# Kernel optimization log

Measured on AMD Instinct MI355X. Metric: run time of the kernel, lower is better.

## Reference

```python
import jax, jax.numpy as jnp
import numpy as np

N = 100000   # nodes per type
E = 400000   # edges per relation
D = 128      # in_dim == out_dim
H = 4        # heads
DK = D // H  # 32
EPS = 1e-5


def setup_inputs() -> dict:
    key = jax.random.key(0)
    ks = jax.random.split(key, 16)
    s = 1.0 / np.sqrt(D)  # fan-in scaling for stable activations
    inp = {
        "x_drug": jax.random.normal(ks[0], (N, D), jnp.float32),
        "x_dis": jax.random.normal(ks[1], (N, D), jnp.float32),
        "Wp_drug": jax.random.normal(ks[2], (D, D), jnp.float32) * s,
        "bp_drug": jnp.zeros((D,), jnp.float32),
        "Wp_dis": jax.random.normal(ks[3], (D, D), jnp.float32) * s,
        "bp_dis": jnp.zeros((D,), jnp.float32),
        "Wk_r0": jax.random.normal(ks[4], (D, D), jnp.float32) * s,
        "Wv_r0": jax.random.normal(ks[5], (D, D), jnp.float32) * s,
        "Wk_r1": jax.random.normal(ks[6], (D, D), jnp.float32) * s,
        "Wv_r1": jax.random.normal(ks[7], (D, D), jnp.float32) * s,
        "Wu_drug": jax.random.normal(ks[8], (D, D), jnp.float32) * s,
        "bu_drug": jnp.zeros((D,), jnp.float32),
        "Wu_dis": jax.random.normal(ks[9], (D, D), jnp.float32) * s,
        "bu_dis": jnp.zeros((D,), jnp.float32),
        "g_drug": jnp.ones((D,), jnp.float32),
        "be_drug": jnp.zeros((D,), jnp.float32),
        "g_dis": jnp.ones((D,), jnp.float32),
        "be_dis": jnp.zeros((D,), jnp.float32),
        "ei_r0": jax.random.randint(ks[10], (2, E), 0, N, jnp.int32),  # drug -> dis
        "ei_r1": jax.random.randint(ks[11], (2, E), 0, N, jnp.int32),  # dis  -> drug
    }
    return inp


def _rel_attention(h_src_all, h_dst_all, ei, Wk, Wv, n_dst):
    # gather -> per-relation K/V proj -> edge softmax over dst -> scatter-add
    src, dst = ei[0], ei[1]
    h_src = h_src_all[src]                                  # [E, D]
    Q = h_dst_all[dst].reshape(-1, H, DK)                   # [E, H, DK]
    K = (h_src @ Wk).reshape(-1, H, DK)
    V = (h_src @ Wv).reshape(-1, H, DK)
    scores = jnp.sum(Q * K, axis=-1) / np.sqrt(DK)          # [E, H]
    # scatter_softmax over destination groups (numerically stable)
    m = jax.lax.stop_gradient(
        jax.ops.segment_max(scores, dst, num_segments=n_dst))  # [N, H]
    ex = jnp.exp(scores - m[dst])
    ssum = jax.ops.segment_sum(ex, dst, num_segments=n_dst)    # [N, H]
    attn = ex / ssum[dst]                                      # [E, H]
    wV = (V * attn[..., None]).reshape(-1, D)                  # [E, D]
    return jax.ops.segment_sum(wV, dst, num_segments=n_dst)    # [N, D]


def _update(h, agg, Wu, bu, g, be):
    x = h + (agg @ Wu + bu)  # skip + update (dropout=0)
    mu = jnp.mean(x, axis=-1, keepdims=True)
    var = jnp.var(x, axis=-1, keepdims=True)
    ln = (x - mu) * jax.lax.rsqrt(var + EPS) * g + be
    return jax.nn.relu(ln)


def reference(x_drug, x_dis, Wp_drug, bp_drug, Wp_dis, bp_dis,
              Wk_r0, Wv_r0, Wk_r1, Wv_r1,
              Wu_drug, bu_drug, Wu_dis, bu_dis,
              g_drug, be_drug, g_dis, be_dis, ei_r0, ei_r1):
    # type-specific projection
    h_drug = x_drug @ Wp_drug + bp_drug
    h_dis = x_dis @ Wp_dis + bp_dis
    # per-relation attention + intra/inter-type aggregation
    agg_dis = _rel_attention(h_drug, h_dis, ei_r0, Wk_r0, Wv_r0, N)
    agg_drug = _rel_attention(h_dis, h_drug, ei_r1, Wk_r1, Wv_r1, N)
    out_drug = _update(h_drug, agg_drug, Wu_drug, bu_drug, g_drug, be_drug)
    out_dis = _update(h_dis, agg_dis, Wu_dis, bu_dis, g_dis, be_dis)
    return jnp.stack([out_drug, out_dis])  # [2, N, D]
```

## Files before the change

### kernel.cpp

```cpp
#include <hip/hip_runtime.h>
#include <math.h>

#define NN 100000
#define EE 400000
#define DD 128

typedef __attribute__((ext_vector_type(8))) short bf16x8;
typedef __attribute__((ext_vector_type(4))) float f32x4;

#if defined(__has_builtin)
#if __has_builtin(__builtin_amdgcn_fdot2_f32_bf16)
#define HAVE_FDOT2 1
typedef __attribute__((ext_vector_type(2))) __bf16 bf16x2t;
#endif
#endif

__device__ __forceinline__ unsigned short f2bf(float f) {
  unsigned u = __float_as_uint(f);
  u += 0x7FFF + ((u >> 16) & 1);
  return (unsigned short)(u >> 16);
}
__device__ __forceinline__ float bf2f(unsigned short u) {
  return __uint_as_float(((unsigned)u) << 16);
}

__global__ __launch_bounds__(256) void prep_weights(
    const float* __restrict__ Wp_dr, const float* __restrict__ bp_dr,
    const float* __restrict__ Wp_di, const float* __restrict__ bp_di,
    const float* __restrict__ Wu_dr, const float* __restrict__ Wu_di,
    const float* __restrict__ Bk0, const float* __restrict__ Bv0,
    const float* __restrict__ Bk1, const float* __restrict__ Bv1,
    unsigned short* __restrict__ Wpt_dr, unsigned short* __restrict__ Wpt_di,
    unsigned short* __restrict__ Wut_dr, unsigned short* __restrict__ Wut_di,
    unsigned short* __restrict__ Wkt0, float* __restrict__ bk0,
    unsigned short* __restrict__ Wvt0, float* __restrict__ bv0,
    unsigned short* __restrict__ Wkt1, float* __restrict__ bk1,
    unsigned short* __restrict__ Wvt1, float* __restrict__ bv1,
    int* __restrict__ deg) {
  const int b = blockIdx.x, t = threadIdx.x;
  if (b < 256) {
    const int id = b * 256 + t;
    const int m = id >> 14, rem = id & 16383, k = rem & 127, c = rem >> 7;
    const float* W = (m == 0) ? Wp_dr : (m == 1) ? Wp_di : (m == 2) ? Wu_dr : Wu_di;
    unsigned short* O = (m == 0) ? Wpt_dr : (m == 1) ? Wpt_di : (m == 2) ? Wut_dr : Wut_di;
    O[c * DD + k] = f2bf(W[(size_t)k * DD + c]);
  } else if (b < 512) {
    const int id = (b - 256) * 256 + t;
    const int m = id >> 14, rem = id & 16383, k = rem & 127, c = rem >> 7;
    const float* A = (m < 2) ? Wp_dr : Wp_di;
    const float* B = (m == 0) ? Bk0 : (m == 1) ? Bv0 : (m == 2) ? Bk1 : Bv1;
    unsigned short* O = (m == 0) ? Wkt0 : (m == 1) ? Wvt0 : (m == 2) ? Wkt1 : Wvt1;
    const float4* a4 = (const float4*)(A + (size_t)k * DD);
    float s = 0.0f;
#pragma unroll 8
    for (int j4 = 0; j4 < 32; ++j4) {
      const float4 av = a4[j4];
      s += av.x * B[(4 * j4 + 0) * DD + c] + av.y * B[(4 * j4 + 1) * DD + c]
         + av.z * B[(4 * j4 + 2) * DD + c] + av.w * B[(4 * j4 + 3) * DD + c];
    }
    O[c * DD + k] = f2bf(s);
  } else if (b < 514) {
    const int id = (b - 512) * 256 + t;
    if (id < 512) {
      const int m = id >> 7, c = id & 127;
      const float* bp = (m < 2) ? bp_dr : bp_di;
      const float* B = (m == 0) ? Bk0 : (m == 1) ? Bv0 : (m == 2) ? Bk1 : Bv1;
      float* bo = (m == 0) ? bk0 : (m == 1) ? bv0 : (m == 2) ? bk1 : bv1;
      float s = 0.0f;
#pragma unroll 8
      for (int j = 0; j < DD; ++j) s += bp[j] * B[j * DD + c];
      bo[c] = s;
    }
  } else {
    const int id = (b - 514) * 256 + t;
    if (id < 2 * NN) deg[id] = 0;
  }
}

#define STAGE_W(SRC)                                                          \
  do {                                                                        \
    __syncthreads();                                                          \
    _Pragma("unroll") for (int i_ = threadIdx.x; i_ < 2048; i_ += 256) {      \
      const int L_ = i_ * 16;                                                 \
      *(float4*)((char*)WL + (L_ ^ (((L_ >> 8) & 15) << 4))) =                \
          ((const float4*)(SRC))[i_];                                         \
    }                                                                         \
    __syncthreads();                                                          \
  } while (0)

__device__ __forceinline__ void mfma_tile_store(
    const unsigned short* WL, const bf16x8* a, int lane, int rowbase,
    bool wvalid, const float* __restrict__ bias,
    unsigned short* __restrict__ outb) {
  const int r0 = rowbase + (lane >> 4) * 4;
#pragma unroll
  for (int ni = 0; ni < 8; ++ni) {
    const int cl = ni * 16 + (lane & 15);
    f32x4 acc = {0.f, 0.f, 0.f, 0.f};
#pragma unroll
    for (int kk = 0; kk < 4; ++kk) {
      const int boff = cl * 256 + ((kk * 64 + (lane >> 4) * 16) ^ ((cl & 15) << 4));
      const bf16x8 bb = *(const bf16x8*)((const char*)WL + boff);
      acc = __builtin_amdgcn_mfma_f32_16x16x32_bf16(a[kk], bb, acc, 0, 0, 0);
    }
    if (wvalid) {
      const float bv = bias[cl];
#pragma unroll
      for (int r = 0; r < 4; ++r)
        outb[(size_t)(r0 + r) * DD + cl] = f2bf(acc[r] + bv);
    }
  }
}

__global__ __launch_bounds__(256) void fused_proj(
    const float* __restrict__ x0, const unsigned short* __restrict__ Wpt0,
    const float* __restrict__ bp0, const unsigned short* __restrict__ Wkta,
    const float* __restrict__ bka, const unsigned short* __restrict__ Wvta,
    const float* __restrict__ bva, unsigned short* __restrict__ h0,
    unsigned short* __restrict__ K0, unsigned short* __restrict__ V0,
    const float* __restrict__ x1, const unsigned short* __restrict__ Wpt1,
    const float* __restrict__ bp1, const unsigned short* __restrict__ Wktb,
    const float* __restrict__ bkb, const unsigned short* __restrict__ Wvtb,
    const float* __restrict__ bvb, unsigned short* __restrict__ h1,
    unsigned short* __restrict__ K1, unsigned short* __restrict__ V1,
    int half, int cntblocks,
    const int* __restrict__ ei0, const int* __restrict__ ei1,
    int* __restrict__ deg) {
  __shared__ unsigned short WL[DD * DD];
  int bid = blockIdx.x;
  if (bid < cntblocks) {
    const int e = bid * 256 + threadIdx.x;
    if (e < 2 * EE) {
      const int d = (e < EE) ? ei0[EE + e] : (NN + ei1[e]);
      atomicAdd(&deg[d], 1);
    }
    return;
  }
  bid -= cntblocks;
  const bool second = bid >= half;
  if (second) bid -= half;
  const float* x = second ? x1 : x0;
  const unsigned short* Wpt = second ? Wpt1 : Wpt0;
  const float* bpv = second ? bp1 : bp0;
  const unsigned short* Wkt = second ? Wktb : Wkta;
  const float* bkv = second ? bkb : bka;
  const unsigned short* Wvt = second ? Wvtb : Wvta;
  const float* bvv = second ? bvb : bva;
  unsigned short* h = second ? h1 : h0;
  unsigned short* K = second ? K1 : K0;
  unsigned short* V = second ? V1 : V0;

  const int tid = threadIdx.x, lane = tid & 63, wid = tid >> 6;
  const int rowbase = bid * 64 + wid * 16;
  const bool wvalid = rowbase < NN;
  bf16x8 a[4];
  if (wvalid) {
    const int arow = rowbase + (lane & 15);
    const float* xr = x + (size_t)arow * DD + (lane >> 4) * 8;
#pragma unroll
    for (int kk = 0; kk < 4; ++kk) {
      const float4 f0 = *(const float4*)(xr + kk * 32);
      const float4 f1 = *(const float4*)(xr + kk * 32 + 4);
      a[kk][0] = (short)f2bf(f0.x); a[kk][1] = (short)f2bf(f0.y);
      a[kk][2] = (short)f2bf(f0.z); a[kk][3] = (short)f2bf(f0.w);
      a[kk][4] = (short)f2bf(f1.x); a[kk][5] = (short)f2bf(f1.y);
      a[kk][6] = (short)f2bf(f1.z); a[kk][7] = (short)f2bf(f1.w);
    }
  } else {
#pragma unroll
    for (int kk = 0; kk < 4; ++kk)
#pragma unroll
      for (int j = 0; j < 8; ++j) a[kk][j] = 0;
  }
  STAGE_W(Wpt);
  mfma_tile_store(WL, a, lane, rowbase, wvalid, bpv, h);
  STAGE_W(Wkt);
  mfma_tile_store(WL, a, lane, rowbase, wvalid, bkv, K);
  STAGE_W(Wvt);
  mfma_tile_store(WL, a, lane, rowbase, wvalid, bvv, V);
}

__global__ __launch_bounds__(256) void update_ln2(
    const unsigned short* __restrict__ hA, const unsigned short* __restrict__ aggA,
    const unsigned short* __restrict__ WutA, const float* __restrict__ buA,
    const float* __restrict__ gA, const float* __restrict__ beA,
    float* __restrict__ outA,
    const unsigned short* __restrict__ hB, const unsigned short* __restrict__ aggB,
    const unsigned short* __restrict__ WutB, const float* __restrict__ buB,
    const float* __restrict__ gB, const float* __restrict__ beB,
    float* __restrict__ outB, int half) {
  __shared__ unsigned short WL[DD * DD];
  int bid = blockIdx.x;
  const bool second = bid >= half;
  if (second) bid -= half;
  const unsigned short* h = second ? hB : hA;
  const unsigned short* agg = second ? aggB : aggA;
  const unsigned short* Wut = second ? WutB : WutA;
  const float* bu = second ? buB : buA;
  const float* g = second ? gB : gA;
  const float* be = second ? beB : beA;
  float* out = second ? outB : outA;

  const int tid = threadIdx.x, lane = tid & 63, wid = tid >> 6;
  const int rowbase = bid * 64 + wid * 16;
  const bool wvalid = rowbase < NN;
  bf16x8 a[4];
  if (wvalid) {
    const int arow = rowbase + (lane & 15);
#pragma unroll
    for (int kk = 0; kk < 4; ++kk)
      a[kk] = *(const bf16x8*)(agg + (size_t)arow * DD + kk * 32 + (lane >> 4) * 8);
  } else {
#pragma unroll
    for (int kk = 0; kk < 4; ++kk)
#pragma unroll
      for (int j = 0; j < 8; ++j) a[kk][j] = 0;
  }
#pragma unroll
  for (int i_ = tid; i_ < 2048; i_ += 256) {
    const int L_ = i_ * 16;
    *(float4*)((char*)WL + (L_ ^ (((L_ >> 8) & 15) << 4))) =
        ((const float4*)Wut)[i_];
  }
  __syncthreads();
  f32x4 acc[8];
  const int r0 = rowbase + (lane >> 4) * 4;
#pragma unroll
  for (int ni = 0; ni < 8; ++ni) {
    const int cl = ni * 16 + (lane & 15);
    acc[ni] = (f32x4){0.f, 0.f, 0.f, 0.f};
#pragma unroll
    for (int kk = 0; kk < 4; ++kk) {
      const int boff = cl * 256 + ((kk * 64 + (lane >> 4) * 16) ^ ((cl & 15) << 4));
      const bf16x8 bb = *(const bf16x8*)((const char*)WL + boff);
      acc[ni] = __builtin_amdgcn_mfma_f32_16x16x32_bf16(a[kk], bb, acc[ni], 0, 0, 0);
    }
  }
  if (!wvalid) return;
#pragma unroll
  for (int ni = 0; ni < 8; ++ni) {
    const int cl = ni * 16 + (lane & 15);
    const float bv = bu[cl];
#pragma unroll
    for (int r = 0; r < 4; ++r)
      acc[ni][r] += bf2f(h[(size_t)(r0 + r) * DD + cl]) + bv;
  }
  float mean[4], inv[4];
#pragma unroll
  for (int r = 0; r < 4; ++r) {
    float s = 0.f, q = 0.f;
#pragma unroll
    for (int ni = 0; ni < 8; ++ni) {
      const float v = acc[ni][r];
      s += v; q += v * v;
    }
    s += __shfl_xor(s, 1); q += __shfl_xor(q, 1);
    s += __shfl_xor(s, 2); q += __shfl_xor(q, 2);
    s += __shfl_xor(s, 4); q += __shfl_xor(q, 4);
    s += __shfl_xor(s, 8); q += __shfl_xor(q, 8);
    const float mu = s * (1.0f / 128.0f);
    mean[r] = mu;
    inv[r] = rsqrtf(q * (1.0f / 128.0f) - mu * mu + 1e-5f);
  }
#pragma unroll
  for (int ni = 0; ni < 8; ++ni) {
    const int cl = ni * 16 + (lane & 15);
    const float gv = g[cl], bev = be[cl];
#pragma unroll
    for (int r = 0; r < 4; ++r)
      out[(size_t)(r0 + r) * DD + cl] =
          fmaxf((acc[ni][r] - mean[r]) * inv[r] * gv + bev, 0.0f);
  }
}

__global__ __launch_bounds__(256) void scan1(const int* __restrict__ deg,
                                             int* __restrict__ excl,
                                             int* __restrict__ partials, int n) {
  __shared__ int ls[256];
  const int b0 = blockIdx.x * 1024;
  const int t = threadIdx.x;
  int v[4];
  int s = 0;
#pragma unroll
  for (int i = 0; i < 4; ++i) {
    const int idx = b0 + t * 4 + i;
    v[i] = (idx < n) ? deg[idx] : 0;
    s += v[i];
  }
  ls[t] = s;
  __syncthreads();
  for (int off = 1; off < 256; off <<= 1) {
    const int x = (t >= off) ? ls[t - off] : 0;
    __syncthreads();
    ls[t] += x;
    __syncthreads();
  }
  int ex = ls[t] - s;
#pragma unroll
  for (int i = 0; i < 4; ++i) {
    const int idx = b0 + t * 4 + i;
    if (idx < n) excl[idx] = ex;
    ex += v[i];
  }
  if (t == 255) partials[blockIdx.x] = ls[255];
}

__global__ __launch_bounds__(256) void scan2(int* __restrict__ partials, int nb) {
  __shared__ int ls[256];
  const int t = threadIdx.x;
  const int v = (t < nb) ? partials[t] : 0;
  ls[t] = v;
  __syncthreads();
  for (int off = 1; off < 256; off <<= 1) {
    const int x = (t >= off) ? ls[t - off] : 0;
    __syncthreads();
    ls[t] += x;
    __syncthreads();
  }
  if (t < nb) partials[t] = ls[t] - v;
}

__global__ __launch_bounds__(256) void scan3(const int* __restrict__ excl,
                                             const int* __restrict__ partials,
                                             int n, int* __restrict__ rowptr) {
  const int i = blockIdx.x * 256 + threadIdx.x;
  if (i < n) rowptr[i] = excl[i] + partials[i >> 10];
}

__global__ __launch_bounds__(256) void fill_csr2(const int* __restrict__ ei0,
                                                 const int* __restrict__ ei1,
                                                 int* __restrict__ rowptr,
                                                 int* __restrict__ csr_src) {
  const int e = blockIdx.x * 256 + threadIdx.x;
  if (e >= 2 * EE) return;
  int s, d;
  if (e < EE) { s = ei0[e]; d = ei0[EE + e]; }
  else        { s = ei1[e - EE]; d = NN + ei1[e]; }
  const int p = atomicAdd(&rowptr[d], 1);
  csr_src[p] = s;
}

__global__ __launch_bounds__(256) void dst_attention(
    const unsigned short* __restrict__ Hq0, const unsigned short* __restrict__ K0,
    const unsigned short* __restrict__ V0, unsigned short* __restrict__ agg0,
    const unsigned short* __restrict__ Hq1, const unsigned short* __restrict__ K1,
    const unsigned short* __restrict__ V1, unsigned short* __restrict__ agg1,
    const int* __restrict__ rowptr, const int* __restrict__ deg,
    const int* __restrict__ csr_src) {
  const int gw = blockIdx.x * 4 + (threadIdx.x >> 6);
  if (gw >= 2 * NN) return;
  const bool rel1 = gw >= NN;
  const int node = rel1 ? gw - NN : gw;
  const unsigned short* Hq = rel1 ? Hq1 : Hq0;
  const char* Kb = (const char*)(rel1 ? K1 : K0);
  const char* Vb = (const char*)(rel1 ? V1 : V0);
  unsigned short* agg = rel1 ? agg1 : agg0;

  const int lane = threadIdx.x & 63;
  const int sub = lane & 15;
  const int grp = lane >> 4;
  const unsigned lboff = (unsigned)sub << 4;
  const int end = rowptr[gw];
  const int beg = end - deg[gw];
  const uint4 qu = *(const uint4*)(Hq + (size_t)node * DD + sub * 8);
#if defined(HAVE_FDOT2)
  const bf16x2t q0 = __builtin_bit_cast(bf16x2t, qu.x);
  const bf16x2t q1 = __builtin_bit_cast(bf16x2t, qu.y);
  const bf16x2t q2 = __builtin_bit_cast(bf16x2t, qu.z);
  const bf16x2t q3 = __builtin_bit_cast(bf16x2t, qu.w);
#else
  float qf[8];
  qf[0] = bf2f((unsigned short)qu.x); qf[1] = bf2f((unsigned short)(qu.x >> 16));
  qf[2] = bf2f((unsigned short)qu.y); qf[3] = bf2f((unsigned short)(qu.y >> 16));
  qf[4] = bf2f((unsigned short)qu.z); qf[5] = bf2f((unsigned short)(qu.z >> 16));
  qf[6] = bf2f((unsigned short)qu.w); qf[7] = bf2f((unsigned short)(qu.w >> 16));
#endif
  float av[8] = {0.f, 0.f, 0.f, 0.f, 0.f, 0.f, 0.f, 0.f};
  float lsum = 0.0f;
  for (int i = beg + grp; i < end; i += 4) {
    const unsigned roff = ((unsigned)csr_src[i] << 8) + lboff;
    const uint4 kp = *(const uint4*)(Kb + roff);
#if defined(HAVE_FDOT2)
    float p = __builtin_amdgcn_fdot2_f32_bf16(__builtin_bit_cast(bf16x2t, kp.x), q0, 0.0f, false);
    p = __builtin_amdgcn_fdot2_f32_bf16(__builtin_bit_cast(bf16x2t, kp.y), q1, p, false);
    p = __builtin_amdgcn_fdot2_f32_bf16(__builtin_bit_cast(bf16x2t, kp.z), q2, p, false);
    p = __builtin_amdgcn_fdot2_f32_bf16(__builtin_bit_cast(bf16x2t, kp.w), q3, p, false);
#else
    float p;
    p  = qf[0] * bf2f((unsigned short)kp.x) + qf[1] * bf2f((unsigned short)(kp.x >> 16));
    p += qf[2] * bf2f((unsigned short)kp.y) + qf[3] * bf2f((unsigned short)(kp.y >> 16));
    p += qf[4] * bf2f((unsigned short)kp.z) + qf[5] * bf2f((unsigned short)(kp.z >> 16));
    p += qf[6] * bf2f((unsigned short)kp.w) + qf[7] * bf2f((unsigned short)(kp.w >> 16));
#endif
    p += __shfl_xor(p, 1);
    p += __shfl_xor(p, 2);
    const float wgt = __expf(p * 0.17677669529663689f);
    const uint4 vp = *(const uint4*)(Vb + roff);
    lsum += wgt;
    av[0] += wgt * __uint_as_float(vp.x << 16);
    av[1] += wgt * __uint_as_float(vp.x & 0xFFFF0000u);
    av[2] += wgt * __uint_as_float(vp.y << 16);
    av[3] += wgt * __uint_as_float(vp.y & 0xFFFF0000u);
    av[4] += wgt * __uint_as_float(vp.z << 16);
    av[5] += wgt * __uint_as_float(vp.z & 0xFFFF0000u);
    av[6] += wgt * __uint_as_float(vp.w << 16);
    av[7] += wgt * __uint_as_float(vp.w & 0xFFFF0000u);
  }
#pragma unroll
  for (int d = 0; d < 8; ++d) {
    av[d] += __shfl_xor(av[d], 16);
    av[d] += __shfl_xor(av[d], 32);
  }
  lsum += __shfl_xor(lsum, 16);
  lsum += __shfl_xor(lsum, 32);
  if (grp == 0) {
    const float invl = (lsum > 0.0f) ? (1.0f / lsum) : 0.0f;
    uint4 o;
    o.x = (unsigned)f2bf(av[0] * invl) | ((unsigned)f2bf(av[1] * invl) << 16);
    o.y = (unsigned)f2bf(av[2] * invl) | ((unsigned)f2bf(av[3] * invl) << 16);
    o.z = (unsigned)f2bf(av[4] * invl) | ((unsigned)f2bf(av[5] * invl) << 16);
    o.w = (unsigned)f2bf(av[6] * invl) | ((unsigned)f2bf(av[7] * invl) << 16);
    *(uint4*)(agg + (size_t)node * DD + sub * 8) = o;
  }
}

extern "C" void kernel_launch(void* const* d_in, const int* in_sizes, int n_in,
                              void* d_out, int out_size, void* d_ws, size_t ws_size,
                              hipStream_t stream) {
  const float* x_drug  = (const float*)d_in[0];
  const float* x_dis   = (const float*)d_in[1];
  const float* Wp_drug = (const float*)d_in[2];
  const float* bp_drug = (const float*)d_in[3];
  const float* Wp_dis  = (const float*)d_in[4];
  const float* bp_dis  = (const float*)d_in[5];
  const float* Wk_r0   = (const float*)d_in[6];
  const float* Wv_r0   = (const float*)d_in[7];
  const float* Wk_r1   = (const float*)d_in[8];
  const float* Wv_r1   = (const float*)d_in[9];
  const float* Wu_drug = (const float*)d_in[10];
  const float* bu_drug = (const float*)d_in[11];
  const float* Wu_dis  = (const float*)d_in[12];
  const float* bu_dis  = (const float*)d_in[13];
  const float* g_drug  = (const float*)d_in[14];
  const float* be_drug = (const float*)d_in[15];
  const float* g_dis   = (const float*)d_in[16];
  const float* be_dis  = (const float*)d_in[17];
  const int* ei_r0     = (const int*)d_in[18];
  const int* ei_r1     = (const int*)d_in[19];

  float* out = (float*)d_out;
  float* out_drug = out;
  float* out_dis  = out + (size_t)NN * DD;

  const size_t ND = (size_t)NN * DD;
  char* w = (char*)d_ws;
  unsigned short* Kr0  = (unsigned short*)w; w += ND * 2;
  unsigned short* Vr0  = (unsigned short*)w; w += ND * 2;
  unsigned short* Kr1  = (unsigned short*)w; w += ND * 2;
  unsigned short* Vr1  = (unsigned short*)w; w += ND * 2;
  unsigned short* agdr = (unsigned short*)w; w += ND * 2;
  unsigned short* agdi = (unsigned short*)w; w += ND * 2;
  unsigned short* hb_dr = (unsigned short*)w; w += ND * 2;
  unsigned short* hb_di = (unsigned short*)w; w += ND * 2;
  unsigned short* Wpt_dr = (unsigned short*)w; w += DD * DD * 2;
  unsigned short* Wpt_di = (unsigned short*)w; w += DD * DD * 2;
  unsigned short* Wut_dr = (unsigned short*)w; w += DD * DD * 2;
  unsigned short* Wut_di = (unsigned short*)w; w += DD * DD * 2;
  unsigned short* Wkt0 = (unsigned short*)w; w += DD * DD * 2;
  unsigned short* Wvt0 = (unsigned short*)w; w += DD * DD * 2;
  unsigned short* Wkt1 = (unsigned short*)w; w += DD * DD * 2;
  unsigned short* Wvt1 = (unsigned short*)w; w += DD * DD * 2;
  float* bk0 = (float*)w; w += DD * 4;
  float* bv0 = (float*)w; w += DD * 4;
  float* bk1 = (float*)w; w += DD * 4;
  float* bv1 = (float*)w; w += DD * 4;
  int* deg      = (int*)w; w += 2 * NN * 4;
  int* excl     = (int*)w; w += 2 * NN * 4;
  int* rowptr   = (int*)w; w += (2 * NN + 1) * 4;
  int* partials = (int*)w; w += 256 * 4;
  int* csr_src  = (int*)w; w += 2 * EE * 4;

  const int gemm_blocks = (NN + 63) / 64;
  const int cnt_blocks = (2 * EE + 255) / 256;
  const int nchunks = (2 * NN + 1023) / 1024;
  const int n256 = (2 * NN + 255) / 256;
  const int attn_blocks = (2 * NN + 3) / 4;
  const int zero_blocks = (2 * NN + 255) / 256;
  dim3 b256(256);

  prep_weights<<<514 + zero_blocks, b256, 0, stream>>>(
      Wp_drug, bp_drug, Wp_dis, bp_dis, Wu_drug, Wu_dis,
      Wk_r0, Wv_r0, Wk_r1, Wv_r1,
      Wpt_dr, Wpt_di, Wut_dr, Wut_di,
      Wkt0, bk0, Wvt0, bv0, Wkt1, bk1, Wvt1, bv1, deg);

  fused_proj<<<cnt_blocks + 2 * gemm_blocks, b256, 0, stream>>>(
      x_drug, Wpt_dr, bp_drug, Wkt0, bk0, Wvt0, bv0, hb_dr, Kr0, Vr0,
      x_dis,  Wpt_di, bp_dis,  Wkt1, bk1, Wvt1, bv1, hb_di, Kr1, Vr1,
      gemm_blocks, cnt_blocks, ei_r0, ei_r1, deg);

  scan1<<<nchunks, b256, 0, stream>>>(deg, excl, partials, 2 * NN);
  scan2<<<1, b256, 0, stream>>>(partials, nchunks);
  scan3<<<n256, b256, 0, stream>>>(excl, partials, 2 * NN, rowptr);
  fill_csr2<<<cnt_blocks, b256, 0, stream>>>(ei_r0, ei_r1, rowptr, csr_src);

  dst_attention<<<attn_blocks, b256, 0, stream>>>(
      hb_di, Kr0, Vr0, agdi,
      hb_dr, Kr1, Vr1, agdr,
      rowptr, deg, csr_src);

  update_ln2<<<2 * gemm_blocks, b256, 0, stream>>>(
      hb_dr, agdr, Wut_dr, bu_drug, g_drug, be_drug, out_drug,
      hb_di, agdi, Wut_di, bu_dis,  g_dis,  be_dis,  out_dis,
      gemm_blocks);
}
```

Baseline: 282.5 us.

## Make projection kernel persistent with all three weights staged once per block

Replaces the one-tile-per-block projection launch with 256 persistent 1024-thread blocks. Each block stages all three bf16 weight matrices (96 KB of LDS) and its bias values once, then loops over 256-row tiles, so the three restaging passes and their barriers per 64-row tile go away. The degree-counting atomics move into a grid-stride loop at the end of the same blocks instead of using separate blocks. The large LDS footprint and 1024-thread blocks limit occupancy to one block per CU, and the fixed 256-block grid may not balance evenly across CUs.

```diff
diff --git a/kernel.cpp b/kernel.cpp
--- a/kernel.cpp
+++ b/kernel.cpp
@@ -4,6 +4,8 @@
 #define NN 100000
 #define EE 400000
 #define DD 128
+#define PB 256
+#define PBH 128
 
 typedef __attribute__((ext_vector_type(8))) short bf16x8;
 typedef __attribute__((ext_vector_type(4))) float f32x4;
@@ -77,21 +79,31 @@
   }
 }
 
-#define STAGE_W(SRC)                                                          \
-  do {                                                                        \
-    __syncthreads();                                                          \
-    _Pragma("unroll") for (int i_ = threadIdx.x; i_ < 2048; i_ += 256) {      \
-      const int L_ = i_ * 16;                                                 \
-      *(float4*)((char*)WL + (L_ ^ (((L_ >> 8) & 15) << 4))) =                \
-          ((const float4*)(SRC))[i_];                                         \
-    }                                                                         \
-    __syncthreads();                                                          \
-  } while (0)
-
-__device__ __forceinline__ void mfma_tile_store(
-    const unsigned short* WL, const bf16x8* a, int lane, int rowbase,
-    bool wvalid, const float* __restrict__ bias,
-    unsigned short* __restrict__ outb) {
+__device__ __forceinline__ void load_xfrag(const float* __restrict__ x,
+                                           int row, bool valid, int lane,
+                                           bf16x8* a) {
+  if (valid) {
+    const float* xr = x + (size_t)row * DD + (lane >> 4) * 8;
+#pragma unroll
+    for (int kk = 0; kk < 4; ++kk) {
+      const float4 f0 = *(const float4*)(xr + kk * 32);
+      const float4 f1 = *(const float4*)(xr + kk * 32 + 4);
+      a[kk][0] = (short)f2bf(f0.x); a[kk][1] = (short)f2bf(f0.y);
+      a[kk][2] = (short)f2bf(f0.z); a[kk][3] = (short)f2bf(f0.w);
+      a[kk][4] = (short)f2bf(f1.x); a[kk][5] = (short)f2bf(f1.y);
+      a[kk][6] = (short)f2bf(f1.z); a[kk][7] = (short)f2bf(f1.w);
+    }
+  } else {
+#pragma unroll
+    for (int kk = 0; kk < 4; ++kk)
+#pragma unroll
+      for (int j = 0; j < 8; ++j) a[kk][j] = 0;
+  }
+}
+
+__device__ __forceinline__ void mfma_tile_store_p(
+    const unsigned short* WLw, const bf16x8* a, int lane, int rowbase,
+    bool wvalid, const float* bias8, unsigned short* __restrict__ outb) {
   const int r0 = rowbase + (lane >> 4) * 4;
 #pragma unroll
   for (int ni = 0; ni < 8; ++ni) {
@@ -100,11 +112,11 @@
 #pragma unroll
     for (int kk = 0; kk < 4; ++kk) {
       const int boff = cl * 256 + ((kk * 64 + (lane >> 4) * 16) ^ ((cl & 15) << 4));
-      const bf16x8 bb = *(const bf16x8*)((const char*)WL + boff);
+      const bf16x8 bb = *(const bf16x8*)((const char*)WLw + boff);
       acc = __builtin_amdgcn_mfma_f32_16x16x32_bf16(a[kk], bb, acc, 0, 0, 0);
     }
     if (wvalid) {
-      const float bv = bias[cl];
+      const float bv = bias8[ni];
 #pragma unroll
       for (int r = 0; r < 4; ++r)
         outb[(size_t)(r0 + r) * DD + cl] = f2bf(acc[r] + bv);
@@ -112,7 +124,7 @@
   }
 }
 
-__global__ __launch_bounds__(256) void fused_proj(
+__global__ __launch_bounds__(1024) void fused_proj(
     const float* __restrict__ x0, const unsigned short* __restrict__ Wpt0,
     const float* __restrict__ bp0, const unsigned short* __restrict__ Wkta,
     const float* __restrict__ bka, const unsigned short* __restrict__ Wvta,
@@ -123,61 +135,63 @@
     const float* __restrict__ bkb, const unsigned short* __restrict__ Wvtb,
     const float* __restrict__ bvb, unsigned short* __restrict__ h1,
     unsigned short* __restrict__ K1, unsigned short* __restrict__ V1,
-    int half, int cntblocks,
     const int* __restrict__ ei0, const int* __restrict__ ei1,
     int* __restrict__ deg) {
-  __shared__ unsigned short WL[DD * DD];
-  int bid = blockIdx.x;
-  if (bid < cntblocks) {
-    const int e = bid * 256 + threadIdx.x;
-    if (e < 2 * EE) {
-      const int d = (e < EE) ? ei0[EE + e] : (NN + ei1[e]);
-      atomicAdd(&deg[d], 1);
-    }
-    return;
-  }
-  bid -= cntblocks;
-  const bool second = bid >= half;
-  if (second) bid -= half;
+  __shared__ unsigned short WL[3 * DD * DD];
+  const int bid = blockIdx.x;
+  const bool second = bid >= PBH;
+  const int tb = second ? bid - PBH : bid;
   const float* x = second ? x1 : x0;
-  const unsigned short* Wpt = second ? Wpt1 : Wpt0;
-  const float* bpv = second ? bp1 : bp0;
-  const unsigned short* Wkt = second ? Wktb : Wkta;
-  const float* bkv = second ? bkb : bka;
-  const unsigned short* Wvt = second ? Wvtb : Wvta;
-  const float* bvv = second ? bvb : bva;
-  unsigned short* h = second ? h1 : h0;
-  unsigned short* K = second ? K1 : K0;
-  unsigned short* V = second ? V1 : V0;
+  const unsigned short* Ws0 = second ? Wpt1 : Wpt0;
+  const unsigned short* Ws1 = second ? Wktb : Wkta;
+  const unsigned short* Ws2 = second ? Wvtb : Wvta;
+  const float* bs0 = second ? bp1 : bp0;
+  const float* bs1 = second ? bkb : bka;
+  const float* bs2 = second ? bvb : bva;
+  unsigned short* out0 = second ? h1 : h0;
+  unsigned short* out1 = second ? K1 : K0;
+  unsigned short* out2 = second ? V1 : V0;
 
   const int tid = threadIdx.x, lane = tid & 63, wid = tid >> 6;
-  const int rowbase = bid * 64 + wid * 16;
-  const bool wvalid = rowbase < NN;
-  bf16x8 a[4];
-  if (wvalid) {
-    const int arow = rowbase + (lane & 15);
-    const float* xr = x + (size_t)arow * DD + (lane >> 4) * 8;
-#pragma unroll
-    for (int kk = 0; kk < 4; ++kk) {
-      const float4 f0 = *(const float4*)(xr + kk * 32);
-      const float4 f1 = *(const float4*)(xr + kk * 32 + 4);
-      a[kk][0] = (short)f2bf(f0.x); a[kk][1] = (short)f2bf(f0.y);
-      a[kk][2] = (short)f2bf(f0.z); a[kk][3] = (short)f2bf(f0.w);
-      a[kk][4] = (short)f2bf(f1.x); a[kk][5] = (short)f2bf(f1.y);
-      a[kk][6] = (short)f2bf(f1.z); a[kk][7] = (short)f2bf(f1.w);
-    }
-  } else {
-#pragma unroll
-    for (int kk = 0; kk < 4; ++kk)
-#pragma unroll
-      for (int j = 0; j < 8; ++j) a[kk][j] = 0;
-  }
-  STAGE_W(Wpt);
-  mfma_tile_store(WL, a, lane, rowbase, wvalid, bpv, h);
-  STAGE_W(Wkt);
-  mfma_tile_store(WL, a, lane, rowbase, wvalid, bkv, K);
-  STAGE_W(Wvt);
-  mfma_tile_store(WL, a, lane, rowbase, wvalid, bvv, V);
+  {
+    const float4* s0 = (const float4*)Ws0;
+    const float4* s1 = (const float4*)Ws1;
+    const float4* s2 = (const float4*)Ws2;
+#pragma unroll
+    for (int i = 0; i < 2; ++i) {
+      const int idx = tid + i * 1024;
+      const int L = idx * 16;
+      const int Ls = L ^ (((L >> 8) & 15) << 4);
+      *(float4*)((char*)WL + Ls) = s0[idx];
+      *(float4*)((char*)(WL + DD * DD) + Ls) = s1[idx];
+      *(float4*)((char*)(WL + 2 * DD * DD) + Ls) = s2[idx];
+    }
+  }
+  float b8a[8], b8b[8], b8c[8];
+#pragma unroll
+  for (int ni = 0; ni < 8; ++ni) {
+    const int cl = ni * 16 + (lane & 15);
+    b8a[ni] = bs0[cl];
+    b8b[ni] = bs1[cl];
+    b8c[ni] = bs2[cl];
+  }
+  __syncthreads();
+
+  const int nrt = (NN + 255) / 256;
+  for (int rt = tb; rt < nrt; rt += PBH) {
+    const int rowbase = rt * 256 + wid * 16;
+    const bool wvalid = rowbase < NN;
+    bf16x8 a[4];
+    load_xfrag(x, rowbase + (lane & 15), wvalid, lane, a);
+    mfma_tile_store_p(WL, a, lane, rowbase, wvalid, b8a, out0);
+    mfma_tile_store_p(WL + DD * DD, a, lane, rowbase, wvalid, b8b, out1);
+    mfma_tile_store_p(WL + 2 * DD * DD, a, lane, rowbase, wvalid, b8c, out2);
+  }
+
+  for (int e = bid * 1024 + tid; e < 2 * EE; e += PB * 1024) {
+    const int d = (e < EE) ? ei0[EE + e] : (NN + ei1[e]);
+    atomicAdd(&deg[d], 1);
+  }
 }
 
 __global__ __launch_bounds__(256) void update_ln2(
@@ -486,7 +500,7 @@
   const int n256 = (2 * NN + 255) / 256;
   const int attn_blocks = (2 * NN + 3) / 4;
   const int zero_blocks = (2 * NN + 255) / 256;
-  dim3 b256(256);
+  dim3 b256(256), b1024(1024);
 
   prep_weights<<<514 + zero_blocks, b256, 0, stream>>>(
       Wp_drug, bp_drug, Wp_dis, bp_dis, Wu_drug, Wu_dis,
@@ -494,10 +508,10 @@
       Wpt_dr, Wpt_di, Wut_dr, Wut_di,
       Wkt0, bk0, Wvt0, bv0, Wkt1, bk1, Wvt1, bv1, deg);
 
-  fused_proj<<<cnt_blocks + 2 * gemm_blocks, b256, 0, stream>>>(
+  fused_proj<<<PB, b1024, 0, stream>>>(
       x_drug, Wpt_dr, bp_drug, Wkt0, bk0, Wvt0, bv0, hb_dr, Kr0, Vr0,
       x_dis,  Wpt_di, bp_dis,  Wkt1, bk1, Wvt1, bv1, hb_di, Kr1, Vr1,
-      gemm_blocks, cnt_blocks, ei_r0, ei_r1, deg);
+      ei_r0, ei_r1, deg);
 
   scan1<<<nchunks, b256, 0, stream>>>(deg, excl, partials, 2 * NN);
   scan2<<<1, b256, 0, stream>>>(partials, nchunks);
```

New measurement: 714.2 us. +152.8%, slower.
